# Kernel tuning notes

Measured on AMD Instinct MI355X. Metric: run time of the kernel, lower is better.

## Reference

```python
import jax, jax.numpy as jnp
import numpy as np

N_NODES = 50000
N_EDGES = 1600000
N_INPUT = 256
HID = 32
OUT = N_INPUT // 2
EPS = 1e-12


def gcn_conv(x, edge_index, W, b):
    # Standard GCNConv: D^{-1/2} (A + I) D^{-1/2} X W + b
    N = x.shape[0]
    loop = jnp.arange(N)
    src = jnp.concatenate([edge_index[0], loop])
    dst = jnp.concatenate([edge_index[1], loop])
    deg = jax.ops.segment_sum(jnp.ones_like(src, dtype=x.dtype), dst, num_segments=N)
    dinv = jax.lax.rsqrt(jnp.maximum(deg, 1.0))  # deg >= 1 due to self-loops
    norm = dinv[src] * dinv[dst]                  # [E+N]
    h = x @ W                                     # [N, out]
    msg = h[src] * norm[:, None]                  # gather + scale
    out = jax.ops.segment_sum(msg, dst, num_segments=N)
    return out + b


def l2_normalize(z):
    n = jnp.linalg.norm(z, axis=1, keepdims=True)
    return z / jnp.maximum(n, EPS)


def setup_inputs() -> dict:
    key = jax.random.key(0)
    ks = jax.random.split(key, 9)
    x = jax.random.normal(ks[0], (N_NODES, N_INPUT), dtype=jnp.float32)
    ei_u = jax.random.randint(ks[1], (2, N_EDGES), 0, N_NODES)
    ei_u2 = jax.random.randint(ks[2], (2, N_EDGES), 0, N_NODES)
    s_in = 1.0 / np.sqrt(N_INPUT)
    s_hid = 1.0 / np.sqrt(HID)
    W_in = jax.random.normal(ks[3], (N_INPUT, HID), dtype=jnp.float32) * s_in
    b_in = jnp.zeros((HID,), dtype=jnp.float32)
    W_hid = jax.random.normal(ks[4], (HID, HID), dtype=jnp.float32) * s_hid
    b_hid = jnp.zeros((HID,), dtype=jnp.float32)
    W_out = jax.random.normal(ks[5], (HID, OUT), dtype=jnp.float32) * s_hid
    b_out = jnp.zeros((OUT,), dtype=jnp.float32)
    return {"x": x, "edge_index_u": ei_u, "edge_index_u2": ei_u2,
            "W_in": W_in, "b_in": b_in, "W_hid": W_hid, "b_hid": b_hid,
            "W_out": W_out, "b_out": b_out}


def reference(x, edge_index_u, edge_index_u2, W_in, b_in, W_hid, b_hid, W_out, b_out):
    # layer 1 on both views
    x1 = gcn_conv(x, edge_index_u, W_in, b_in)
    x2 = gcn_conv(x, edge_index_u2, W_in, b_in)
    sim = jnp.sum(l2_normalize(x1) * l2_normalize(x2), axis=1, keepdims=True)
    mian = x1 + x2 * sim
    sup = x2 + x1 * sim
    # layer 2
    x1 = gcn_conv(mian, edge_index_u, W_hid, b_hid)
    x2 = gcn_conv(sup, edge_index_u2, W_hid, b_hid)
    sim = jnp.sum(l2_normalize(x1) * l2_normalize(x2), axis=1, keepdims=True)
    mian = x1 + x2 * sim
    sup = x2 + x1 * sim
    # layer 3: note both branches use edge_index_u (as in source)
    x1 = gcn_conv(mian, edge_index_u, W_out, b_out)
    x2 = gcn_conv(sup, edge_index_u, W_out, b_out)
    return jnp.concatenate([x1, x2], axis=1)
```

## Files before the change

### kernel.cpp

```cpp
#include <hip/hip_runtime.h>
#include <hip/hip_bf16.h>

#define NN 50000
#define NE 1600000
#define NIN 256
#define HID 32
#define FOUT 128
#define OSTR 256
#define NSB ((NN + 255) / 256)
#define CHUNK 2048
#define NCH ((NE + CHUNK - 1) / CHUNK)

static constexpr float EPS = 1e-12f;

__device__ __forceinline__ float b2f(unsigned short s) {
    return __uint_as_float((unsigned)s << 16);
}
__device__ __forceinline__ unsigned short f2b(float f) {
    unsigned u = __float_as_uint(f);
    u += 0x7FFFu + ((u >> 16) & 1u);
    return (unsigned short)(u >> 16);
}
__device__ __forceinline__ unsigned pack2(float a, float b) {
    return (unsigned)f2b(a) | ((unsigned)f2b(b) << 16);
}

__global__ __launch_bounds__(256) void k_hist(const int* __restrict__ dstA,
                                              const int* __restrict__ dstB,
                                              unsigned* __restrict__ hcA,
                                              unsigned* __restrict__ hcB, int half) {
    __shared__ unsigned h[NSB];
    for (int i = threadIdx.x; i < NSB; i += 256) h[i] = 0u;
    __syncthreads();
    bool sec = blockIdx.x >= half;
    int c = sec ? blockIdx.x - half : blockIdx.x;
    const int* dst = sec ? dstB : dstA;
    unsigned* hc = sec ? hcB : hcA;
    int beg = c * CHUNK, end = min(beg + CHUNK, NE);
    for (int e = beg + (int)threadIdx.x; e < end; e += 256)
        atomicAdd(&h[dst[e] >> 8], 1u);
    __syncthreads();
    for (int i = threadIdx.x; i < NSB; i += 256) hc[(size_t)c * NSB + i] = h[i];
}

__global__ __launch_bounds__(256) void k_cscan(unsigned* __restrict__ hcA,
                                               unsigned* __restrict__ hcB,
                                               unsigned* __restrict__ totA,
                                               unsigned* __restrict__ totB, int half) {
    __shared__ unsigned tile[256];
    __shared__ unsigned carry;
    bool sec = blockIdx.x >= half;
    int sb = sec ? blockIdx.x - half : blockIdx.x;
    unsigned* hc = sec ? hcB : hcA;
    unsigned* tot = sec ? totB : totA;
    if (threadIdx.x == 0) carry = 0u;
    __syncthreads();
    for (int base = 0; base < NCH; base += 256) {
        int c = base + (int)threadIdx.x;
        unsigned v = (c < NCH) ? hc[(size_t)c * NSB + sb] : 0u;
        tile[threadIdx.x] = v;
        __syncthreads();
        for (int off = 1; off < 256; off <<= 1) {
            unsigned t = (threadIdx.x >= (unsigned)off) ? tile[threadIdx.x - off] : 0u;
            __syncthreads();
            tile[threadIdx.x] += t;
            __syncthreads();
        }
        if (c < NCH) hc[(size_t)c * NSB + sb] = carry + tile[threadIdx.x] - v;
        __syncthreads();
        if (threadIdx.x == 0) carry += tile[255];
        __syncthreads();
    }
    if (threadIdx.x == 0) tot[sb] = carry;
}

__global__ __launch_bounds__(256) void k_bscan(const unsigned* __restrict__ totA,
                                               const unsigned* __restrict__ totB,
                                               int* __restrict__ bbA, int* __restrict__ bbB) {
    __shared__ unsigned tile[256];
    const unsigned* tot = blockIdx.x ? totB : totA;
    int* bb = blockIdx.x ? bbB : bbA;
    unsigned v = (threadIdx.x < NSB) ? tot[threadIdx.x] : 0u;
    tile[threadIdx.x] = v;
    __syncthreads();
    for (int off = 1; off < 256; off <<= 1) {
        unsigned t = (threadIdx.x >= (unsigned)off) ? tile[threadIdx.x - off] : 0u;
        __syncthreads();
        tile[threadIdx.x] += t;
        __syncthreads();
    }
    if (threadIdx.x < NSB) bb[threadIdx.x] = (int)(tile[threadIdx.x] - v);
    if (threadIdx.x == 0) bb[NSB] = NE;
}

__global__ __launch_bounds__(256) void k_bin1(const int* __restrict__ srcA,
                                              const int* __restrict__ dstA,
                                              const unsigned* __restrict__ hcA,
                                              const int* __restrict__ bbA,
                                              int* __restrict__ tmpA,
                                              const int* __restrict__ srcB,
                                              const int* __restrict__ dstB,
                                              const unsigned* __restrict__ hcB,
                                              const int* __restrict__ bbB,
                                              int* __restrict__ tmpB, int half) {
    __shared__ unsigned hbase[NSB];
    __shared__ unsigned hcur[NSB];
    __shared__ unsigned hscan[NSB];
    __shared__ unsigned tile[256];
    __shared__ unsigned pay[CHUNK];
    __shared__ unsigned gpos[CHUNK];
    bool sec = blockIdx.x >= half;
    int c = sec ? blockIdx.x - half : blockIdx.x;
    const int* src = sec ? srcB : srcA;
    const int* dst = sec ? dstB : dstA;
    const unsigned* hc = sec ? hcB : hcA;
    const int* bb = sec ? bbB : bbA;
    int* tmp = sec ? tmpB : tmpA;
    for (int i = threadIdx.x; i < NSB; i += 256) {
        hbase[i] = (unsigned)bb[i] + hc[(size_t)c * NSB + i];
        hcur[i] = 0u;
    }
    __syncthreads();
    int beg = c * CHUNK;
    int len = min(CHUNK, NE - beg);
    int d[8], s[8];
#pragma unroll
    for (int j = 0; j < 8; ++j) {
        int idx = j * 256 + (int)threadIdx.x;
        if (idx < len) { d[j] = dst[beg + idx]; s[j] = src[beg + idx]; }
        else d[j] = -1;
    }
#pragma unroll
    for (int j = 0; j < 8; ++j)
        if (d[j] >= 0) atomicAdd(&hcur[d[j] >> 8], 1u);
    __syncthreads();
    unsigned v = (threadIdx.x < NSB) ? hcur[threadIdx.x] : 0u;
    tile[threadIdx.x] = v;
    __syncthreads();
    for (int off = 1; off < 256; off <<= 1) {
        unsigned t = (threadIdx.x >= (unsigned)off) ? tile[threadIdx.x - off] : 0u;
        __syncthreads();
        tile[threadIdx.x] += t;
        __syncthreads();
    }
    if (threadIdx.x < NSB) {
        unsigned excl = tile[threadIdx.x] - v;
        hscan[threadIdx.x] = excl;
        hcur[threadIdx.x] = excl;
    }
    __syncthreads();
#pragma unroll
    for (int j = 0; j < 8; ++j) {
        if (d[j] >= 0) {
            int sb = d[j] >> 8;
            unsigned p = atomicAdd(&hcur[sb], 1u);
            pay[p] = ((unsigned)(d[j] & 255) << 16) | (unsigned)s[j];
            gpos[p] = hbase[sb] + (p - hscan[sb]);
        }
    }
    __syncthreads();
    for (int i = threadIdx.x; i < len; i += 256)
        tmp[gpos[i]] = (int)pay[i];
}

__global__ __launch_bounds__(256) void k_bin2(const int* __restrict__ tmpA,
                                              const int* __restrict__ bbA,
                                              unsigned short* __restrict__ csrA,
                                              unsigned* __restrict__ degA,
                                              float* __restrict__ dinvA,
                                              int* __restrict__ rpA,
                                              const int* __restrict__ tmpB,
                                              const int* __restrict__ bbB,
                                              unsigned short* __restrict__ csrB,
                                              unsigned* __restrict__ degB,
                                              float* __restrict__ dinvB,
                                              int* __restrict__ rpB, int half) {
    __shared__ unsigned cnt[256];
    __shared__ unsigned scan[256];
    __shared__ unsigned curs[256];
    bool sec = blockIdx.x >= half;
    int sb = sec ? blockIdx.x - half : blockIdx.x;
    const int* tmp = sec ? tmpB : tmpA;
    const int* bb = sec ? bbB : bbA;
    unsigned short* csr = sec ? csrB : csrA;
    unsigned* deg = sec ? degB : degA;
    float* dinv = sec ? dinvB : dinvA;
    int* rp = sec ? rpB : rpA;
    int beg = bb[sb], end = bb[sb + 1];
    cnt[threadIdx.x] = 0u;
    __syncthreads();
    for (int e = beg + (int)threadIdx.x; e < end; e += 256)
        atomicAdd(&cnt[(tmp[e] >> 16) & 255], 1u);
    __syncthreads();
    unsigned v = cnt[threadIdx.x];
    scan[threadIdx.x] = v;
    __syncthreads();
    for (int off = 1; off < 256; off <<= 1) {
        unsigned t = (threadIdx.x >= (unsigned)off) ? scan[threadIdx.x - off] : 0u;
        __syncthreads();
        scan[threadIdx.x] += t;
        __syncthreads();
    }
    unsigned excl = scan[threadIdx.x] - v;
    int n = sb * 256 + (int)threadIdx.x;
    if (n < NN) {
        deg[n] = v;
        rp[n] = beg + (int)excl;
        dinv[n] = rsqrtf((float)(v + 1u));
    }
    curs[threadIdx.x] = (unsigned)beg + excl;
    __syncthreads();
    for (int e = beg + (int)threadIdx.x; e < end; e += 256) {
        int p = tmp[e];
        unsigned pos = atomicAdd(&curs[(p >> 16) & 255], 1u);
        csr[pos] = (unsigned short)(p & 0xFFFF);
    }
}

__global__ __launch_bounds__(512) void k_gemm_in(const float* __restrict__ x,
                                                 const float* __restrict__ W,
                                                 const float* __restrict__ dinvU,
                                                 const float* __restrict__ dinvV,
                                                 unsigned short* __restrict__ hU,
                                                 unsigned short* __restrict__ hV, int N) {
    int lane = threadIdx.x & 63;
    int c0 = __builtin_amdgcn_readfirstlane((int)(threadIdx.x >> 6) * 4);
    int row = blockIdx.x * 64 + lane;
    if (row >= N) return;
    const float4* xr = reinterpret_cast<const float4*>(x + (size_t)row * NIN);
    float acc[4] = {0.f, 0.f, 0.f, 0.f};
#pragma unroll 4
    for (int k4 = 0; k4 < NIN / 4; ++k4) {
        float4 v = xr[k4];
        const float* Wk = W + k4 * 4 * HID + c0;
#pragma unroll
        for (int j = 0; j < 4; ++j) {
            acc[j] = fmaf(v.x, Wk[j], acc[j]);
            acc[j] = fmaf(v.y, Wk[HID + j], acc[j]);
            acc[j] = fmaf(v.z, Wk[2 * HID + j], acc[j]);
            acc[j] = fmaf(v.w, Wk[3 * HID + j], acc[j]);
        }
    }
    float du = dinvU[row], dw = dinvV[row];
    uint2 wu, wv;
    wu.x = pack2(acc[0] * du, acc[1] * du); wu.y = pack2(acc[2] * du, acc[3] * du);
    wv.x = pack2(acc[0] * dw, acc[1] * dw); wv.y = pack2(acc[2] * dw, acc[3] * dw);
    *reinterpret_cast<uint2*>(hU + (size_t)row * HID + c0) = wu;
    *reinterpret_cast<uint2*>(hV + (size_t)row * HID + c0) = wv;
}

__device__ __forceinline__ void pull_sum(const unsigned short* __restrict__ t,
                                         const unsigned short* __restrict__ csr,
                                         const int* __restrict__ rowptr,
                                         const unsigned* __restrict__ deg,
                                         float* __restrict__ out, int blk, int tid) {
    int node = blk * 32 + tid / 8;
    int q = tid % 8;
    if (node >= NN) return;
    const ushort4* h4 = reinterpret_cast<const ushort4*>(t);
    int beg = rowptr[node];
    int end = beg + (int)deg[node];
    ushort4 sv = h4[(size_t)node * 8 + q];
    float4 acc;
    acc.x = b2f(sv.x); acc.y = b2f(sv.y); acc.z = b2f(sv.z); acc.w = b2f(sv.w);
    int e = beg;
    for (; e + 4 <= end; e += 4) {
        int s0 = csr[e], s1 = csr[e + 1], s2 = csr[e + 2], s3 = csr[e + 3];
        ushort4 v0 = h4[(size_t)s0 * 8 + q];
        ushort4 v1 = h4[(size_t)s1 * 8 + q];
        ushort4 v2 = h4[(size_t)s2 * 8 + q];
        ushort4 v3 = h4[(size_t)s3 * 8 + q];
        acc.x += (b2f(v0.x) + b2f(v1.x)) + (b2f(v2.x) + b2f(v3.x));
        acc.y += (b2f(v0.y) + b2f(v1.y)) + (b2f(v2.y) + b2f(v3.y));
        acc.z += (b2f(v0.z) + b2f(v1.z)) + (b2f(v2.z) + b2f(v3.z));
        acc.w += (b2f(v0.w) + b2f(v1.w)) + (b2f(v2.w) + b2f(v3.w));
    }
    for (; e < end; ++e) {
        ushort4 v0 = h4[(size_t)csr[e] * 8 + q];
        acc.x += b2f(v0.x); acc.y += b2f(v0.y);
        acc.z += b2f(v0.z); acc.w += b2f(v0.w);
    }
    *reinterpret_cast<float4*>(out + (size_t)node * HID + q * 4) = acc;
}

__global__ __launch_bounds__(256) void k_pull_pair(
    const unsigned short* __restrict__ tA, const unsigned short* __restrict__ csrA,
    const int* __restrict__ rpA, const unsigned* __restrict__ degA, float* __restrict__ outA,
    const unsigned short* __restrict__ tB, const unsigned short* __restrict__ csrB,
    const int* __restrict__ rpB, const unsigned* __restrict__ degB, float* __restrict__ outB,
    int nblk) {
    int b = blockIdx.x;
    int xcd = b & 7;
    int blk = (b >> 3) * 4 + (xcd & 3);
    if (blk >= nblk) return;
    if (xcd >= 4) pull_sum(tB, csrB, rpB, degB, outB, blk, threadIdx.x);
    else          pull_sum(tA, csrA, rpA, degA, outA, blk, threadIdx.x);
}

__global__ __launch_bounds__(256) void k_mix1(const float* __restrict__ Su,
                                              const float* __restrict__ Sv,
                                              const float* __restrict__ dinvU,
                                              const float* __restrict__ dinvV,
                                              const float* __restrict__ bias,
                                              unsigned short* __restrict__ Tu,
                                              unsigned short* __restrict__ Tv) {
    int node = blockIdx.x * 32 + (threadIdx.x >> 3);
    int q = threadIdx.x & 7;
    if (node >= NN) return;
    float4 su = *reinterpret_cast<const float4*>(Su + (size_t)node * HID + 4 * q);
    float4 sv = *reinterpret_cast<const float4*>(Sv + (size_t)node * HID + 4 * q);
    float du = dinvU[node], dw = dinvV[node];
    float a0 = fmaf(su.x, du, bias[4 * q + 0]);
    float a1 = fmaf(su.y, du, bias[4 * q + 1]);
    float a2 = fmaf(su.z, du, bias[4 * q + 2]);
    float a3 = fmaf(su.w, du, bias[4 * q + 3]);
    float b0 = fmaf(sv.x, dw, bias[4 * q + 0]);
    float b1 = fmaf(sv.y, dw, bias[4 * q + 1]);
    float b2 = fmaf(sv.z, dw, bias[4 * q + 2]);
    float b3 = fmaf(sv.w, dw, bias[4 * q + 3]);
    float n1 = a0 * a0 + a1 * a1 + a2 * a2 + a3 * a3;
    float n2 = b0 * b0 + b1 * b1 + b2 * b2 + b3 * b3;
    float dt = a0 * b0 + a1 * b1 + a2 * b2 + a3 * b3;
#pragma unroll
    for (int m = 4; m >= 1; m >>= 1) {
        n1 += __shfl_xor(n1, m);
        n2 += __shfl_xor(n2, m);
        dt += __shfl_xor(dt, m);
    }
    float sim = dt / (fmaxf(sqrtf(n1), EPS) * fmaxf(sqrtf(n2), EPS));
    uint2 mu, mv;
    mu.x = pack2((a0 + b0 * sim) * du, (a1 + b1 * sim) * du);
    mu.y = pack2((a2 + b2 * sim) * du, (a3 + b3 * sim) * du);
    mv.x = pack2((b0 + a0 * sim) * dw, (b1 + a1 * sim) * dw);
    mv.y = pack2((b2 + a2 * sim) * dw, (b3 + a3 * sim) * dw);
    *reinterpret_cast<uint2*>(Tu + (size_t)node * HID + 4 * q) = mu;
    *reinterpret_cast<uint2*>(Tv + (size_t)node * HID + 4 * q) = mv;
}

__global__ __launch_bounds__(256) void k_hid_mix_pack(const float* __restrict__ Su,
                                                      const float* __restrict__ Sv,
                                                      const float* __restrict__ W,
                                                      const float* __restrict__ bias,
                                                      const float* __restrict__ dinvU,
                                                      const float* __restrict__ dinvV,
                                                      unsigned short* __restrict__ Pa,
                                                      unsigned short* __restrict__ Pb) {
    __shared__ float Ws[HID * HID];
    __shared__ float zu[32][33];
    __shared__ float zv[32][33];
    int t = threadIdx.x;
    for (int i = t; i < HID * HID; i += 256) Ws[i] = W[i];
    int nb = blockIdx.x * 32;
    int l = t >> 3, q = t & 7;
    int node = nb + l;
    {
        float4 fu = make_float4(0.f, 0.f, 0.f, 0.f), fv = fu;
        if (node < NN) {
            fu = *reinterpret_cast<const float4*>(Su + (size_t)node * HID + 4 * q);
            fv = *reinterpret_cast<const float4*>(Sv + (size_t)node * HID + 4 * q);
        }
        zu[l][4 * q + 0] = fu.x; zu[l][4 * q + 1] = fu.y;
        zu[l][4 * q + 2] = fu.z; zu[l][4 * q + 3] = fu.w;
        zv[l][4 * q + 0] = fv.x; zv[l][4 * q + 1] = fv.y;
        zv[l][4 * q + 2] = fv.z; zv[l][4 * q + 3] = fv.w;
    }
    __syncthreads();
    if (node >= NN) return;
    float a[4] = {0.f, 0.f, 0.f, 0.f};
    float b[4] = {0.f, 0.f, 0.f, 0.f};
#pragma unroll
    for (int k = 0; k < HID; ++k) {
        float zuk = zu[l][k], zvk = zv[l][k];
        const float* Wk = Ws + k * HID + 4 * q;
#pragma unroll
        for (int j = 0; j < 4; ++j) {
            a[j] = fmaf(zuk, Wk[j], a[j]);
            b[j] = fmaf(zvk, Wk[j], b[j]);
        }
    }
    float du = dinvU[node], dw = dinvV[node];
#pragma unroll
    for (int j = 0; j < 4; ++j) {
        a[j] = fmaf(a[j], du, bias[4 * q + j]);
        b[j] = fmaf(b[j], dw, bias[4 * q + j]);
    }
    float n1 = a[0]*a[0] + a[1]*a[1] + a[2]*a[2] + a[3]*a[3];
    float n2 = b[0]*b[0] + b[1]*b[1] + b[2]*b[2] + b[3]*b[3];
    float dt = a[0]*b[0] + a[1]*b[1] + a[2]*b[2] + a[3]*b[3];
#pragma unroll
    for (int m = 4; m >= 1; m >>= 1) {
        n1 += __shfl_xor(n1, m);
        n2 += __shfl_xor(n2, m);
        dt += __shfl_xor(dt, m);
    }
    float sim = dt / (fmaxf(sqrtf(n1), EPS) * fmaxf(sqrtf(n2), EPS));
    uint2 ma, mb;
    ma.x = pack2((a[0] + b[0] * sim) * du, (a[1] + b[1] * sim) * du);
    ma.y = pack2((a[2] + b[2] * sim) * du, (a[3] + b[3] * sim) * du);
    mb.x = pack2((b[0] + a[0] * sim) * du, (b[1] + a[1] * sim) * du);
    mb.y = pack2((b[2] + a[2] * sim) * du, (b[3] + a[3] * sim) * du);
    *reinterpret_cast<uint2*>(Pa + (size_t)node * HID + 4 * q) = ma;
    *reinterpret_cast<uint2*>(Pb + (size_t)node * HID + 4 * q) = mb;
}

__global__ __launch_bounds__(512) void k_gemm_out2(const float* __restrict__ Qa,
                                                   const float* __restrict__ Qb,
                                                   const float* __restrict__ dinvU,
                                                   const float* __restrict__ W,
                                                   const float* __restrict__ b,
                                                   float* __restrict__ out, int N) {
    int lane = threadIdx.x & 63;
    int wv = (int)(threadIdx.x >> 6);
    int view = __builtin_amdgcn_readfirstlane(wv >> 2);
    int c0 = __builtin_amdgcn_readfirstlane((wv & 3) * 32);
    int row = blockIdx.x * 64 + lane;
    if (row >= N) return;
    const float* Q = view ? Qb : Qa;
    const float4* q4 = reinterpret_cast<const float4*>(Q + (size_t)row * HID);
    float a[32];
#pragma unroll
    for (int j = 0; j < 32; ++j) a[j] = 0.f;
#pragma unroll 2
    for (int k4 = 0; k4 < 8; ++k4) {
        float4 v = q4[k4];
        const float* Wk = W + (k4 * 4) * FOUT + c0;
#pragma unroll
        for (int j = 0; j < 32; ++j) {
            a[j] = fmaf(v.x, Wk[j], a[j]);
            a[j] = fmaf(v.y, Wk[FOUT + j], a[j]);
            a[j] = fmaf(v.z, Wk[2 * FOUT + j], a[j]);
            a[j] = fmaf(v.w, Wk[3 * FOUT + j], a[j]);
        }
    }
    float du = dinvU[row];
    float* o = out + (size_t)row * OSTR + view * FOUT + c0;
#pragma unroll
    for (int g = 0; g < 8; ++g) {
        float4 r;
        r.x = fmaf(a[4*g+0], du, b[c0+4*g+0]);
        r.y = fmaf(a[4*g+1], du, b[c0+4*g+1]);
        r.z = fmaf(a[4*g+2], du, b[c0+4*g+2]);
        r.w = fmaf(a[4*g+3], du, b[c0+4*g+3]);
        *reinterpret_cast<float4*>(o + 4 * g) = r;
    }
}

extern "C" void kernel_launch(void* const* d_in, const int* in_sizes, int n_in,
                              void* d_out, int out_size, void* d_ws, size_t ws_size,
                              hipStream_t stream) {
    const float* x     = (const float*)d_in[0];
    const int*   ei_u  = (const int*)d_in[1];
    const int*   ei_u2 = (const int*)d_in[2];
    const float* W_in  = (const float*)d_in[3];
    const float* b_in  = (const float*)d_in[4];
    const float* W_hid = (const float*)d_in[5];
    const float* b_hid = (const float*)d_in[6];
    const float* W_out = (const float*)d_in[7];
    const float* b_out = (const float*)d_in[8];
    float* out = (float*)d_out;

    const int* src_u  = ei_u;
    const int* dst_u  = ei_u + NE;
    const int* src_u2 = ei_u2;
    const int* dst_u2 = ei_u2 + NE;

    char* w = (char*)d_ws;
    auto carve = [&](size_t bytes) {
        char* p = w;
        w += (bytes + 255) & ~(size_t)255;
        return p;
    };
    unsigned* hc_u   = (unsigned*)carve((size_t)NCH * NSB * sizeof(unsigned));
    unsigned* hc_u2  = (unsigned*)carve((size_t)NCH * NSB * sizeof(unsigned));
    unsigned* tot_u  = (unsigned*)carve(NSB * sizeof(unsigned));
    unsigned* tot_u2 = (unsigned*)carve(NSB * sizeof(unsigned));
    int*      bb_u   = (int*)carve((NSB + 1) * sizeof(int));
    int*      bb_u2  = (int*)carve((NSB + 1) * sizeof(int));
    unsigned* deg_u  = (unsigned*)carve(NN * sizeof(unsigned));
    unsigned* deg_u2 = (unsigned*)carve(NN * sizeof(unsigned));
    float*    dinv_u  = (float*)carve(NN * sizeof(float));
    float*    dinv_u2 = (float*)carve(NN * sizeof(float));
    int*      rp_u   = (int*)carve(NN * sizeof(int));
    int*      rp_u2  = (int*)carve(NN * sizeof(int));
    unsigned short* csr_u  = (unsigned short*)carve((size_t)NE * sizeof(unsigned short));
    unsigned short* csr_u2 = (unsigned short*)carve((size_t)NE * sizeof(unsigned short));
    unsigned short* hU = (unsigned short*)carve((size_t)NN * HID * sizeof(unsigned short));
    unsigned short* hV = (unsigned short*)carve((size_t)NN * HID * sizeof(unsigned short));
    unsigned short* Tu = (unsigned short*)carve((size_t)NN * HID * sizeof(unsigned short));
    unsigned short* Tv = (unsigned short*)carve((size_t)NN * HID * sizeof(unsigned short));
    unsigned short* Pa = (unsigned short*)carve((size_t)NN * HID * sizeof(unsigned short));
    unsigned short* Pb = (unsigned short*)carve((size_t)NN * HID * sizeof(unsigned short));
    float* Su = (float*)carve((size_t)NN * HID * sizeof(float));
    float* Sv = (float*)carve((size_t)NN * HID * sizeof(float));
    int* tmp_u  = (int*)Su;
    int* tmp_u2 = (int*)Sv;

    const int BLK = 256;
    const int gP32 = (NN + 31) / 32;
    const int nPair = ((gP32 + 3) / 4) * 8;
    const int gR64 = (NN + 63) / 64;

    k_hist<<<2 * NCH, BLK, 0, stream>>>(dst_u, dst_u2, hc_u, hc_u2, NCH);
    k_cscan<<<2 * NSB, BLK, 0, stream>>>(hc_u, hc_u2, tot_u, tot_u2, NSB);
    k_bscan<<<2, BLK, 0, stream>>>(tot_u, tot_u2, bb_u, bb_u2);
    k_bin1<<<2 * NCH, BLK, 0, stream>>>(src_u, dst_u, hc_u, bb_u, tmp_u,
                                        src_u2, dst_u2, hc_u2, bb_u2, tmp_u2, NCH);
    k_bin2<<<2 * NSB, BLK, 0, stream>>>(tmp_u, bb_u, csr_u, deg_u, dinv_u, rp_u,
                                        tmp_u2, bb_u2, csr_u2, deg_u2, dinv_u2, rp_u2, NSB);

    k_gemm_in<<<gR64, 512, 0, stream>>>(x, W_in, dinv_u, dinv_u2, hU, hV, NN);
    k_pull_pair<<<nPair, BLK, 0, stream>>>(hU, csr_u, rp_u, deg_u, Su,
                                           hV, csr_u2, rp_u2, deg_u2, Sv, gP32);
    k_mix1<<<gP32, BLK, 0, stream>>>(Su, Sv, dinv_u, dinv_u2, b_in, Tu, Tv);

    k_pull_pair<<<nPair, BLK, 0, stream>>>(Tu, csr_u, rp_u, deg_u, Su,
                                           Tv, csr_u2, rp_u2, deg_u2, Sv, gP32);
    k_hid_mix_pack<<<gP32, BLK, 0, stream>>>(Su, Sv, W_hid, b_hid, dinv_u, dinv_u2, Pa, Pb);

    k_pull_pair<<<nPair, BLK, 0, stream>>>(Pa, csr_u, rp_u, deg_u, Su,
                                           Pb, csr_u, rp_u, deg_u, Sv, gP32);
    k_gemm_out2<<<gR64, 512, 0, stream>>>(Su, Sv, dinv_u, W_out, b_out, out, NN);

    (void)in_sizes; (void)n_in; (void)out_size; (void)ws_size;
}
```

Baseline: 247.2 us.

## Split input GEMM over K across waves with LDS reduction

The input projection kernel now gives each wave a quarter of the K dimension and all 32 output columns, instead of all of K and only 4 columns. Each row of x is therefore read once rather than eight times across waves. Partial sums go through shared memory and are reduced before packing to bf16 with the two degree scalings. The cost is 32 accumulators per thread, a 33 KB LDS buffer and a block barrier, which may lower occupancy.

Result: faster. 208.9 us (-15.5%).

```diff
diff --git a/kernel.cpp b/kernel.cpp
--- a/kernel.cpp
+++ b/kernel.cpp
@@ -217,36 +217,59 @@
     }
 }
 
-__global__ __launch_bounds__(512) void k_gemm_in(const float* __restrict__ x,
+__global__ __launch_bounds__(256) void k_gemm_in(const float* __restrict__ x,
                                                  const float* __restrict__ W,
                                                  const float* __restrict__ dinvU,
                                                  const float* __restrict__ dinvV,
                                                  unsigned short* __restrict__ hU,
                                                  unsigned short* __restrict__ hV, int N) {
+    __shared__ float part[4 * 64 * 33];
     int lane = threadIdx.x & 63;
-    int c0 = __builtin_amdgcn_readfirstlane((int)(threadIdx.x >> 6) * 4);
+    int wv = __builtin_amdgcn_readfirstlane((int)(threadIdx.x >> 6));
     int row = blockIdx.x * 64 + lane;
-    if (row >= N) return;
-    const float4* xr = reinterpret_cast<const float4*>(x + (size_t)row * NIN);
-    float acc[4] = {0.f, 0.f, 0.f, 0.f};
+    float acc[32];
+#pragma unroll
+    for (int j = 0; j < 32; ++j) acc[j] = 0.f;
+    if (row < N) {
+        const float4* xr = reinterpret_cast<const float4*>(x + (size_t)row * NIN);
 #pragma unroll 4
-    for (int k4 = 0; k4 < NIN / 4; ++k4) {
-        float4 v = xr[k4];
-        const float* Wk = W + k4 * 4 * HID + c0;
-#pragma unroll
-        for (int j = 0; j < 4; ++j) {
-            acc[j] = fmaf(v.x, Wk[j], acc[j]);
-            acc[j] = fmaf(v.y, Wk[HID + j], acc[j]);
-            acc[j] = fmaf(v.z, Wk[2 * HID + j], acc[j]);
-            acc[j] = fmaf(v.w, Wk[3 * HID + j], acc[j]);
+        for (int i = 0; i < 16; ++i) {
+            int k4 = wv * 16 + i;
+            float4 v = xr[k4];
+            const float* Wk = W + k4 * 4 * HID;
+#pragma unroll
+            for (int j = 0; j < 32; ++j) {
+                acc[j] = fmaf(v.x, Wk[j], acc[j]);
+                acc[j] = fmaf(v.y, Wk[HID + j], acc[j]);
+                acc[j] = fmaf(v.z, Wk[2 * HID + j], acc[j]);
+                acc[j] = fmaf(v.w, Wk[3 * HID + j], acc[j]);
+            }
         }
     }
-    float du = dinvU[row], dw = dinvV[row];
-    uint2 wu, wv;
-    wu.x = pack2(acc[0] * du, acc[1] * du); wu.y = pack2(acc[2] * du, acc[3] * du);
-    wv.x = pack2(acc[0] * dw, acc[1] * dw); wv.y = pack2(acc[2] * dw, acc[3] * dw);
-    *reinterpret_cast<uint2*>(hU + (size_t)row * HID + c0) = wu;
-    *reinterpret_cast<uint2*>(hV + (size_t)row * HID + c0) = wv;
+    float* pw = part + (wv * 64 + lane) * 33;
+#pragma unroll
+    for (int j = 0; j < 32; ++j) pw[j] = acc[j];
+    __syncthreads();
+    int r = threadIdx.x >> 2;
+    int c0 = (threadIdx.x & 3) * 8;
+    int orow = blockIdx.x * 64 + r;
+    if (orow >= N) return;
+    float s[8];
+#pragma unroll
+    for (int i = 0; i < 8; ++i) {
+        s[i] = part[(0 * 64 + r) * 33 + c0 + i]
+             + part[(1 * 64 + r) * 33 + c0 + i]
+             + part[(2 * 64 + r) * 33 + c0 + i]
+             + part[(3 * 64 + r) * 33 + c0 + i];
+    }
+    float du = dinvU[orow], dw = dinvV[orow];
+    uint4 wu, wvv;
+    wu.x = pack2(s[0] * du, s[1] * du); wu.y = pack2(s[2] * du, s[3] * du);
+    wu.z = pack2(s[4] * du, s[5] * du); wu.w = pack2(s[6] * du, s[7] * du);
+    wvv.x = pack2(s[0] * dw, s[1] * dw); wvv.y = pack2(s[2] * dw, s[3] * dw);
+    wvv.z = pack2(s[4] * dw, s[5] * dw); wvv.w = pack2(s[6] * dw, s[7] * dw);
+    *reinterpret_cast<uint4*>(hU + (size_t)orow * HID + c0) = wu;
+    *reinterpret_cast<uint4*>(hV + (size_t)orow * HID + c0) = wvv;
 }
 
 __device__ __forceinline__ void pull_sum(const unsigned short* __restrict__ t,
@@ -508,7 +531,7 @@
     k_bin2<<<2 * NSB, BLK, 0, stream>>>(tmp_u, bb_u, csr_u, deg_u, dinv_u, rp_u,
                                         tmp_u2, bb_u2, csr_u2, deg_u2, dinv_u2, rp_u2, NSB);
 
-    k_gemm_in<<<gR64, 512, 0, stream>>>(x, W_in, dinv_u, dinv_u2, hU, hV, NN);
+    k_gemm_in<<<gR64, BLK, 0, stream>>>(x, W_in, dinv_u, dinv_u2, hU, hV, NN);
     k_pull_pair<<<nPair, BLK, 0, stream>>>(hU, csr_u, rp_u, deg_u, Su,
                                            hV, csr_u2, rp_u2, deg_u2, Sv, gP32);
     k_mix1<<<gP32, BLK, 0, stream>>>(Su, Sv, dinv_u, dinv_u2, b_in, Tu, Tv);
```
